# Kernel optimization log

Hardware: AMD Instinct MI355X
Metric: run time of the kernel (lower is better)

The kernel has to match this reference:

```python
import jax, jax.numpy as jnp
import numpy as np

# Dimensions matching init_kwargs
B, T, F = 256, 512, 128
COH_PTS, BULK_PTS, OUT_LEN = 64, 128, 6
COH_SIZE = 2 * COH_PTS            # fc11 out
IN_BULK = F + COH_PTS             # fc12 in
BULK_SIZE = 3 * BULK_PTS          # fc12 out

# Material constants (Turon cohesive bilinear law + J2 plasticity w/ linear hardening)
DELTA0, DELTAF = 0.01, 0.1        # damage onset / final equivalent jump
E_MOD, NU = 1.0e3, 0.3
G_MOD = E_MOD / (2.0 * (1.0 + NU))
SIG_Y, HARD = 10.0, 100.0
EPS = 1e-12
LEAKY_SLOPE = 0.01


def _plane_stress_D():
    c = E_MOD / (1.0 - NU * NU)
    return jnp.array([[c, c * NU, 0.0],
                      [c * NU, c, 0.0],
                      [0.0, 0.0, c * (1.0 - NU) / 2.0]], dtype=jnp.float32)


def setup_inputs() -> dict:
    key = jax.random.key(0)
    k_x, k_w11, k_b11, k_w12, k_w2 = jax.random.split(key, 5)
    scale11 = 1.0 / np.sqrt(F)
    scale12 = 1.0 / np.sqrt(IN_BULK)
    scale2 = 1.0 / np.sqrt(BULK_SIZE)
    return {
        "x": jax.random.normal(k_x, (B, T, F), dtype=jnp.float32),
        "W11": jax.random.normal(k_w11, (COH_SIZE, F), dtype=jnp.float32) * scale11,
        "b11": jax.random.normal(k_b11, (COH_SIZE,), dtype=jnp.float32) * scale11,
        "W12": jax.random.normal(k_w12, (BULK_SIZE, IN_BULK), dtype=jnp.float32) * scale12,
        "W2": jax.random.normal(k_w2, (OUT_LEN, BULK_SIZE), dtype=jnp.float32) * scale2,
    }


def reference(x, W11, b11, W12, W2):
    b, t, f = x.shape
    coh_pts = W11.shape[0] // 2
    bulk_pts = W12.shape[0] // 3
    D = _plane_stress_D()

    # fc11 (leaky-relu linear) is history-free -> vectorize over all timesteps
    jumps = jax.nn.leaky_relu(jnp.einsum('btf,cf->btc', x, W11) + b11,
                              LEAKY_SLOPE).reshape(b, t, coh_pts, 2)

    def step(carry, inp):
        dmg, ep = carry                      # [b, coh_pts], [b, bulk_pts]
        x_t, jump_t = inp                    # [b, f], [b, coh_pts, 2]

        # --- Turon cohesive update: monotone bilinear damage on equivalent jump ---
        jn = jax.nn.relu(jump_t[..., 0])     # tension-only normal jump
        js = jump_t[..., 1]
        delta = jnp.sqrt(jn * jn + js * js + EPS)
        d_new = jnp.clip(DELTAF * (delta - DELTA0)
                         / (jnp.maximum(delta, EPS) * (DELTAF - DELTA0)), 0.0, 1.0)
        dmg = jnp.maximum(dmg, d_new)        # commit: damage never heals

        # --- midini = cat(input, damages) -> fc12 (no bias) ---
        midini = jnp.concatenate([x_t, dmg], axis=-1)          # [b, f+coh_pts]
        strain = (midini @ W12.T).reshape(b, bulk_pts, 3)       # [b, bulk_pts, 3]

        # --- J2 plasticity (plane stress, radial return, linear hardening) ---
        sig_tr = jnp.einsum('bpi,ji->bpj', strain, D)           # trial stress
        sxx, syy, txy = sig_tr[..., 0], sig_tr[..., 1], sig_tr[..., 2]
        seq = jnp.sqrt(sxx * sxx - sxx * syy + syy * syy + 3.0 * txy * txy + EPS)
        fyield = seq - (SIG_Y + HARD * ep)
        dep = jnp.where(fyield > 0.0, fyield / (3.0 * G_MOD + HARD), 0.0)
        ep = ep + dep                                           # commit history
        scale = jnp.where(fyield > 0.0, (SIG_Y + HARD * ep) / seq, 1.0)
        sig = sig_tr * scale[..., None]

        # --- fc2 (softLayer: linear no bias + softplus) ---
        out_t = jax.nn.softplus(sig.reshape(b, -1) @ W2.T)      # [b, out_len]
        return (dmg, ep), out_t

    carry0 = (jnp.zeros((b, coh_pts), jnp.float32),
              jnp.zeros((b, bulk_pts), jnp.float32))
    _, out = jax.lax.scan(step, carry0,
                          (jnp.swapaxes(x, 0, 1), jnp.swapaxes(jumps, 0, 1)))
    return jnp.swapaxes(out, 0, 1)           # [b, t, out_len]
```

## Files before the change

kernel.cpp:

```cpp
#include <hip/hip_runtime.h>
#include <hip/hip_bf16.h>
#include <math.h>

#define NB 256
#define NT 512
#define NF 128
#define NCOH 64
#define NIN 192
#define NBS 384
#define NROWS (NB*NT)

#define C11 1098.9010989010989f
#define C12 329.67032967032966f
#define C33 384.61538461538464f
#define H3G 1253.8461538461538f
#define HOVER 0.07975460122699386f

typedef __attribute__((ext_vector_type(8))) short bf16x8;
typedef __attribute__((ext_vector_type(4))) float f32x4;
typedef __attribute__((ext_vector_type(8))) unsigned short ushort8v;
typedef __attribute__((ext_vector_type(4))) unsigned short ushort4v;

#define WAITCNT_VM(N) __builtin_amdgcn_s_waitcnt(0x0F70 | ((N) & 15) | (((N) >> 4) << 14))

#define PS ((size_t)NROWS * 32)
__device__ unsigned short g_Ahi[6 * PS];
__device__ unsigned short g_Bres[2 * NBS * NIN];
__device__ unsigned short g_W11res[32768];

static __device__ __forceinline__ unsigned short f2bf(float v) {
    __hip_bfloat16 h = __float2bfloat16(v);
    return *reinterpret_cast<unsigned short*>(&h);
}
static __device__ __forceinline__ float bf2f(unsigned short u) {
    unsigned int x = ((unsigned int)u) << 16;
    return *reinterpret_cast<float*>(&x);
}
static __device__ __forceinline__ void async_copy16(const void* g, void* l) {
    __builtin_amdgcn_global_load_lds(
        (const __attribute__((address_space(1))) unsigned int*)g,
        (__attribute__((address_space(3))) unsigned int*)l, 16, 0, 0);
}

__global__ __launch_bounds__(256) void k0_w12(const float* __restrict__ W12)
{
    const int idx = blockIdx.x * 256 + threadIdx.x;
    const int e    = idx & 7;
    const int l    = (idx >> 3) & 63;
    const int nf   = (idx >> 9) & 3;
    const int part = (idx >> 11) & 1;
    const int kc   = (idx >> 12) % 6;
    const int nblk = idx / 24576;
    const int n = nblk * 64 + nf * 16 + (l & 15);
    const int k = kc * 32 + (l >> 4) * 8 + e;
    const int p = n / 3, j = n - 3 * p;
    const float* w = W12 + (size_t)(3 * p) * NIN;
    float v;
    if (j == 0)      v = C11 * w[k]           + C12 * w[NIN + k];
    else if (j == 1) v = C12 * w[k]           + C11 * w[NIN + k];
    else             v = C33 * w[2 * NIN + k];
    unsigned short h = f2bf(v);
    g_Bres[idx] = part ? f2bf(v - bf2f(h)) : h;
}

__global__ __launch_bounds__(256) void k0b_w11(const float* __restrict__ W11)
{
    const int idx = blockIdx.x * 256 + threadIdx.x;
    const int e    = idx & 7;
    const int l    = (idx >> 3) & 63;
    const int nf   = (idx >> 9) & 7;
    const int part = (idx >> 12) & 1;
    const int kc   = idx >> 13;
    const int n = nf * 16 + (l & 15);
    const int k = kc * 32 + (l >> 4) * 8 + e;
    const float v = W11[(size_t)n * NF + k];
    unsigned short h = f2bf(v);
    g_W11res[idx] = part ? f2bf(v - bf2f(h)) : h;
}

__global__ __launch_bounds__(256) void k1_fc11(
    const float* __restrict__ x, const float* __restrict__ b11,
    unsigned short* __restrict__ dnT)
{
    __shared__ unsigned short Ws[32768];

    const int tid = threadIdx.x;
    const int lane = tid & 63, w = tid >> 6;
    const int fr = lane & 15, fq = lane >> 4;
    const int xbase = blockIdx.x * 128 + w * 32;

#pragma unroll
    for (int i = 0; i < 16; ++i)
        async_copy16((const char*)g_W11res + tid * 16 + i * 4096,
                     (char*)Ws + tid * 16 + i * 4096);

    f32x4 acc[8][2];
#pragma unroll
    for (int q = 0; q < 8; ++q)
#pragma unroll
        for (int f = 0; f < 2; ++f) acc[q][f] = (f32x4){0.f, 0.f, 0.f, 0.f};

    WAITCNT_VM(0);
    __builtin_amdgcn_s_barrier();

#pragma unroll
    for (int kc = 0; kc < 4; ++kc) {
        bf16x8 ah[2], al[2];
#pragma unroll
        for (int f = 0; f < 2; ++f) {
            const int row = xbase + f * 16 + fr;
            const float* xs = x + (size_t)row * NF + kc * 32 + fq * 8;
            float4 v0 = ((const float4*)xs)[0];
            float4 v1 = ((const float4*)xs)[1];
            float v[8] = {v0.x, v0.y, v0.z, v0.w, v1.x, v1.y, v1.z, v1.w};
            ushort8v h, lo;
#pragma unroll
            for (int i = 0; i < 8; ++i) {
                h[i]  = f2bf(v[i]);
                lo[i] = f2bf(v[i] - bf2f(h[i]));
            }
            *(ushort8v*)(g_Ahi + (size_t)kc * PS + (size_t)row * 32 + fq * 8) = h;
            ah[f] = *reinterpret_cast<bf16x8*>(&h);
            al[f] = *reinterpret_cast<bf16x8*>(&lo);
        }
#pragma unroll
        for (int q = 0; q < 8; ++q) {
            bf16x8 wh = *(const bf16x8*)&Ws[(kc * 16 + q) * 512 + lane * 8];
            bf16x8 wl = *(const bf16x8*)&Ws[(kc * 16 + 8 + q) * 512 + lane * 8];
#pragma unroll
            for (int f = 0; f < 2; ++f) {
                acc[q][f] = __builtin_amdgcn_mfma_f32_16x16x32_bf16(
                    wh, ah[f], acc[q][f], 0, 0, 0);
                acc[q][f] = __builtin_amdgcn_mfma_f32_16x16x32_bf16(
                    wl, ah[f], acc[q][f], 0, 0, 0);
                acc[q][f] = __builtin_amdgcn_mfma_f32_16x16x32_bf16(
                    wh, al[f], acc[q][f], 0, 0, 0);
            }
        }
    }

#pragma unroll
    for (int q = 0; q < 8; ++q) {
        float4 bv = *(const float4*)(b11 + q * 16 + fq * 4);
#pragma unroll
        for (int f = 0; f < 2; ++f) {
            const int xrow = xbase + f * 16 + fr;
            float z[4] = {acc[q][f][0] + bv.x, acc[q][f][1] + bv.y,
                          acc[q][f][2] + bv.z, acc[q][f][3] + bv.w};
#pragma unroll
            for (int pr = 0; pr < 2; ++pr) {
                float jn = fmaxf(z[2 * pr], 0.0f);
                float zs = z[2 * pr + 1];
                float js = (zs > 0.0f) ? zs : 0.01f * zs;
                float delta = sqrtf(jn * jn + js * js + 1e-12f);
                float dn = 0.1f * (delta - 0.01f) / (fmaxf(delta, 1e-12f) * 0.09f);
                dn = fminf(fmaxf(dn, 0.0f), 1.0f);
                dnT[(size_t)(q * 8 + fq * 2 + pr) * NROWS + xrow] = f2bf(dn);
            }
        }
    }
}

__global__ __launch_bounds__(64) void k2a(const unsigned short* __restrict__ dnT,
                                          float* __restrict__ totals)
{
    const int b = blockIdx.x >> 3, seg = blockIdx.x & 7;
    const int c = threadIdx.x;
    const ushort8v* p = (const ushort8v*)(dnT + (size_t)c * NROWS + b * NT + seg * 64);
    float m = 0.0f;
#pragma unroll
    for (int g = 0; g < 8; ++g) {
        ushort8v v = p[g];
#pragma unroll
        for (int i = 0; i < 8; ++i) m = fmaxf(m, bf2f(v[i]));
    }
    totals[(size_t)(b * 8 + seg) * 64 + c] = m;
}

__global__ __launch_bounds__(64) void k2b(const unsigned short* __restrict__ dnT,
                                          const float* __restrict__ totals)
{
    const int b = blockIdx.x >> 3, seg = blockIdx.x & 7;
    const int c = threadIdx.x;
    float carry = 0.0f;
    for (int s = 0; s < seg; ++s)
        carry = fmaxf(carry, totals[(size_t)(b * 8 + s) * 64 + c]);
    const ushort8v* p = (const ushort8v*)(dnT + (size_t)c * NROWS + b * NT + seg * 64);
    unsigned short* ah = g_Ahi + (size_t)(4 + (c >> 5)) * PS
                       + (size_t)(b * NT + seg * 64) * 32 + (c & 31);
    float m = carry;
#pragma unroll
    for (int g = 0; g < 8; ++g) {
        ushort8v v = p[g];
#pragma unroll
        for (int i = 0; i < 8; ++i) {
            m = fmaxf(m, bf2f(v[i]));
            ah[(size_t)(g * 8 + i) * 32] = f2bf(m);
        }
    }
}

__global__ __launch_bounds__(256, 3) void k3_mfma(unsigned short* __restrict__ sigT)
{
    __shared__ unsigned short Bs[24576];

    const int tid = threadIdx.x;
    const int lane = tid & 63, w = tid >> 6;
    const int id = blockIdx.x;
    const int sw = (id & 7) * 384 + (id >> 3);
    const int nblk = sw % 6;
    const int m0 = (sw / 6) * 256;
    const int n0 = nblk * 64;
    const int wm = w * 64;
    const int fr = lane & 15, fq = lane >> 4;

    const size_t abase = (size_t)(m0 + wm + fr) * 32 + fq * 8;

    bf16x8 a0[4], a1[4];
#pragma unroll
    for (int mi = 0; mi < 4; ++mi)
        a0[mi] = *(const bf16x8*)(g_Ahi + abase + mi * 512);

    {
        const char* bsrc = (const char*)g_Bres + (size_t)nblk * 49152;
#pragma unroll
        for (int i = 0; i < 12; ++i)
            async_copy16(bsrc + tid * 16 + i * 4096, (char*)Bs + tid * 16 + i * 4096);
    }
    WAITCNT_VM(0);
    __builtin_amdgcn_s_barrier();

    f32x4 acc[4][4];
#pragma unroll
    for (int mi = 0; mi < 4; ++mi)
#pragma unroll
        for (int ni = 0; ni < 4; ++ni) acc[mi][ni] = (f32x4){0.f, 0.f, 0.f, 0.f};

#pragma unroll
    for (int c = 0; c < 6; ++c) {
        bf16x8* acur = (c & 1) ? a1 : a0;
        bf16x8* anxt = (c & 1) ? a0 : a1;
        if (c < 5) {
#pragma unroll
            for (int mi = 0; mi < 4; ++mi)
                anxt[mi] = *(const bf16x8*)(g_Ahi + (size_t)(c + 1) * PS
                                            + abase + mi * 512);
        }
        bf16x8 bh[4], bl[4];
#pragma unroll
        for (int ni = 0; ni < 4; ++ni) {
            bh[ni] = *(const bf16x8*)&Bs[((c * 8 + ni) << 9) + lane * 8];
            bl[ni] = *(const bf16x8*)&Bs[((c * 8 + 4 + ni) << 9) + lane * 8];
        }
#pragma unroll
        for (int mi = 0; mi < 4; ++mi)
#pragma unroll
            for (int ni = 0; ni < 4; ++ni) {
                acc[mi][ni] = __builtin_amdgcn_mfma_f32_16x16x32_bf16(
                    acur[mi], bh[ni], acc[mi][ni], 0, 0, 0);
                acc[mi][ni] = __builtin_amdgcn_mfma_f32_16x16x32_bf16(
                    acur[mi], bl[ni], acc[mi][ni], 0, 0, 0);
            }
    }

    const int b_idx = m0 >> 9;
    const int tbase = (m0 & 511) + wm + fq * 4;
#pragma unroll
    for (int mi = 0; mi < 4; ++mi)
#pragma unroll
        for (int ni = 0; ni < 4; ++ni) {
            const int col = n0 + ni * 16 + fr;
            ushort4v h;
#pragma unroll
            for (int r = 0; r < 4; ++r) h[r] = f2bf(acc[mi][ni][r]);
            *(ushort4v*)(sigT + (((size_t)(b_idx * NBS + col)) << 9)
                              + tbase + mi * 16) = h;
        }
}

#define PFD 8
__global__ __launch_bounds__(128) void k4_scan(
    const unsigned short* __restrict__ sigT, unsigned short* __restrict__ uT)
{
    const int b = blockIdx.x;
    const int p = threadIdx.x;
    const ushort8v* sx = (const ushort8v*)(sigT + (((size_t)(b * NBS + 3 * p    )) << 9));
    const ushort8v* sy = (const ushort8v*)(sigT + (((size_t)(b * NBS + 3 * p + 1)) << 9));
    const ushort8v* sz = (const ushort8v*)(sigT + (((size_t)(b * NBS + 3 * p + 2)) << 9));
    ushort8v* uo = (ushort8v*)(uT + (((size_t)(b * 128 + p)) << 9));

    ushort8v px[PFD], py[PFD], pz[PFD];
#pragma unroll
    for (int g = 0; g < PFD; ++g) { px[g] = sx[g]; py[g] = sy[g]; pz[g] = sz[g]; }

    float u = 10.0f;
#pragma unroll 8
    for (int g = 0; g < 64 - PFD; ++g) {
        const int sl = g & (PFD - 1);
        ushort8v vx = px[sl], vy = py[sl], vz = pz[sl];
        px[sl] = sx[g + PFD]; py[sl] = sy[g + PFD]; pz[sl] = sz[g + PFD];
        ushort8v ov;
#pragma unroll
        for (int i = 0; i < 8; ++i) {
            float sxx = bf2f(vx[i]), syy = bf2f(vy[i]), txy = bf2f(vz[i]);
            float e = sxx*sxx - sxx*syy + syy*syy + 3.0f*txy*txy + 1e-12f;
            float seq = sqrtf(e);
            u = fmaf(fmaxf(seq - u, 0.0f), HOVER, u);
            ov[i] = f2bf(u);
        }
        uo[g] = ov;
    }
#pragma unroll
    for (int g = 64 - PFD; g < 64; ++g) {
        const int sl = g & (PFD - 1);
        ushort8v vx = px[sl], vy = py[sl], vz = pz[sl];
        ushort8v ov;
#pragma unroll
        for (int i = 0; i < 8; ++i) {
            float sxx = bf2f(vx[i]), syy = bf2f(vy[i]), txy = bf2f(vz[i]);
            float e = sxx*sxx - sxx*syy + syy*syy + 3.0f*txy*txy + 1e-12f;
            float seq = sqrtf(e);
            u = fmaf(fmaxf(seq - u, 0.0f), HOVER, u);
            ov[i] = f2bf(u);
        }
        uo[g] = ov;
    }
}

__global__ __launch_bounds__(256) void k5_out(
    const unsigned short* __restrict__ sigT, const unsigned short* __restrict__ uT,
    const float* __restrict__ W2, float* __restrict__ out)
{
    __shared__ float W2s[6][NBS];
    const int tid = threadIdx.x;
    for (int i = tid; i < 6 * NBS; i += 256) W2s[i / NBS][i % NBS] = W2[i];
    __syncthreads();

    const int b = blockIdx.x >> 1;
    const int t = (blockIdx.x & 1) * 256 + tid;
    const unsigned short* sb = sigT + (((size_t)b * NBS) << 9) + t;
    const unsigned short* ub = uT + (((size_t)b * 128) << 9) + t;

    float acc[6] = {0, 0, 0, 0, 0, 0};
#pragma unroll 4
    for (int p = 0; p < 128; ++p) {
        float sxx = bf2f(sb[(size_t)(3 * p    ) << 9]);
        float syy = bf2f(sb[(size_t)(3 * p + 1) << 9]);
        float txy = bf2f(sb[(size_t)(3 * p + 2) << 9]);
        float u   = bf2f(ub[(size_t)p << 9]);
        float e = sxx*sxx - sxx*syy + syy*syy + 3.0f*txy*txy + 1e-12f;
        float scale = fminf(1.0f, u * rsqrtf(e));
        float fx = sxx * scale, fy = syy * scale, fz = txy * scale;
#pragma unroll
        for (int o = 0; o < 6; ++o) {
            acc[o] = fmaf(fx, W2s[o][3 * p    ], acc[o]);
            acc[o] = fmaf(fy, W2s[o][3 * p + 1], acc[o]);
            acc[o] = fmaf(fz, W2s[o][3 * p + 2], acc[o]);
        }
    }

    float* op = out + ((size_t)(b * NT + t)) * 6;
#pragma unroll
    for (int o = 0; o < 6; ++o) {
        float z = acc[o];
        op[o] = fmaxf(z, 0.0f) + log1pf(expf(-fabsf(z)));
    }
}

extern "C" void kernel_launch(void* const* d_in, const int* in_sizes, int n_in,
                              void* d_out, int out_size, void* d_ws, size_t ws_size,
                              hipStream_t stream)
{
    const float* x   = (const float*)d_in[0];
    const float* W11 = (const float*)d_in[1];
    const float* b11 = (const float*)d_in[2];
    const float* W12 = (const float*)d_in[3];
    const float* W2  = (const float*)d_in[4];
    float* out = (float*)d_out;

    unsigned short* dnT = (unsigned short*)d_ws;
    unsigned short* uT = (unsigned short*)d_ws;
    unsigned short* sigT = (unsigned short*)((char*)d_ws + (size_t)NROWS * NCOH * sizeof(float));
    float* totals = (float*)((char*)d_ws + (size_t)128 * 1024 * 1024);

    k0_w12<<<(2 * NBS * NIN) / 256, 256, 0, stream>>>(W12);
    k0b_w11<<<128, 256, 0, stream>>>(W11);
    k1_fc11<<<NROWS / 128, 256, 0, stream>>>(x, b11, dnT);
    k2a<<<NB * 8, 64, 0, stream>>>(dnT, totals);
    k2b<<<NB * 8, 64, 0, stream>>>(dnT, totals);
    k3_mfma<<<3072, 256, 0, stream>>>(sigT);
    k4_scan<<<NB, 128, 0, stream>>>(sigT, uT);
    k5_out<<<NROWS / 256, 256, 0, stream>>>(sigT, uT, W2, out);
}
```

Measured before the change: 271.2 us.

## Fuse plasticity scan with output layer and stage GEMM stores through LDS

Merges the scan and output kernels into one 512-thread block per batch. The per-point yield-stress history is kept in a swizzled 128KB LDS buffer instead of being written to and re-read from global memory. The MFMA kernel also transposes its tile through shared memory so each lane writes 16-byte coalesced rows of sigT instead of scattered 8-byte stores. The trade-offs are that only 256 blocks run, the scan uses just 128 of 512 threads while the other 384 wait at the barrier, and W2 is now read from global/cache rather than LDS.

After: 308.1 us. 13.6% more time.

```diff
diff --git a/kernel.cpp b/kernel.cpp
--- a/kernel.cpp
+++ b/kernel.cpp
@@ -263,99 +263,110 @@
             }
     }
 
+    __syncthreads();
+    unsigned short* T = Bs;
+#pragma unroll
+    for (int mi = 0; mi < 4; ++mi)
+#pragma unroll
+        for (int ni = 0; ni < 4; ++ni) {
+            const int cIdx = ni * 16 + fr;
+            const int tloc = wm + mi * 16 + fq * 4;
+            ushort4v h;
+#pragma unroll
+            for (int r = 0; r < 4; ++r) h[r] = f2bf(acc[mi][ni][r]);
+            *(ushort4v*)&T[cIdx * 272 + tloc] = h;
+        }
+    __syncthreads();
+
     const int b_idx = m0 >> 9;
-    const int tbase = (m0 & 511) + wm + fq * 4;
-#pragma unroll
-    for (int mi = 0; mi < 4; ++mi)
-#pragma unroll
-        for (int ni = 0; ni < 4; ++ni) {
-            const int col = n0 + ni * 16 + fr;
-            ushort4v h;
-#pragma unroll
-            for (int r = 0; r < 4; ++r) h[r] = f2bf(acc[mi][ni][r]);
-            *(ushort4v*)(sigT + (((size_t)(b_idx * NBS + col)) << 9)
-                              + tbase + mi * 16) = h;
-        }
+    const int tq = lane & 31, c2 = lane >> 5;
+    const size_t colbase = (((size_t)(b_idx * NBS + n0)) << 9) + (m0 & 511);
+#pragma unroll
+    for (int it = 0; it < 8; ++it) {
+        const int cc = w * 16 + it * 2 + c2;
+        ushort8v v = *(const ushort8v*)&T[cc * 272 + tq * 8];
+        *(ushort8v*)(sigT + colbase + ((size_t)cc << 9) + tq * 8) = v;
+    }
 }
 
 #define PFD 8
-__global__ __launch_bounds__(128) void k4_scan(
-    const unsigned short* __restrict__ sigT, unsigned short* __restrict__ uT)
-{
+__global__ __launch_bounds__(512) void k45(
+    const unsigned short* __restrict__ sigT, const float* __restrict__ W2,
+    float* __restrict__ out)
+{
+    __shared__ unsigned short Ul[512 * 128];
+
+    const int tid = threadIdx.x;
     const int b = blockIdx.x;
-    const int p = threadIdx.x;
-    const ushort8v* sx = (const ushort8v*)(sigT + (((size_t)(b * NBS + 3 * p    )) << 9));
-    const ushort8v* sy = (const ushort8v*)(sigT + (((size_t)(b * NBS + 3 * p + 1)) << 9));
-    const ushort8v* sz = (const ushort8v*)(sigT + (((size_t)(b * NBS + 3 * p + 2)) << 9));
-    ushort8v* uo = (ushort8v*)(uT + (((size_t)(b * 128 + p)) << 9));
-
-    ushort8v px[PFD], py[PFD], pz[PFD];
-#pragma unroll
-    for (int g = 0; g < PFD; ++g) { px[g] = sx[g]; py[g] = sy[g]; pz[g] = sz[g]; }
-
-    float u = 10.0f;
+
+    if (tid < 128) {
+        const int p = tid;
+        const int pc = (p >> 3) << 3;
+        const int pw = p & 7;
+        const ushort8v* sx = (const ushort8v*)(sigT + (((size_t)(b * NBS + 3 * p    )) << 9));
+        const ushort8v* sy = (const ushort8v*)(sigT + (((size_t)(b * NBS + 3 * p + 1)) << 9));
+        const ushort8v* sz = (const ushort8v*)(sigT + (((size_t)(b * NBS + 3 * p + 2)) << 9));
+
+        ushort8v px[PFD], py[PFD], pz[PFD];
+#pragma unroll
+        for (int g = 0; g < PFD; ++g) { px[g] = sx[g]; py[g] = sy[g]; pz[g] = sz[g]; }
+
+        float u = 10.0f;
 #pragma unroll 8
-    for (int g = 0; g < 64 - PFD; ++g) {
-        const int sl = g & (PFD - 1);
-        ushort8v vx = px[sl], vy = py[sl], vz = pz[sl];
-        px[sl] = sx[g + PFD]; py[sl] = sy[g + PFD]; pz[sl] = sz[g + PFD];
-        ushort8v ov;
+        for (int g = 0; g < 64 - PFD; ++g) {
+            const int sl = g & (PFD - 1);
+            ushort8v vx = px[sl], vy = py[sl], vz = pz[sl];
+            px[sl] = sx[g + PFD]; py[sl] = sy[g + PFD]; pz[sl] = sz[g + PFD];
+#pragma unroll
+            for (int i = 0; i < 8; ++i) {
+                float sxx = bf2f(vx[i]), syy = bf2f(vy[i]), txy = bf2f(vz[i]);
+                float e = sxx*sxx - sxx*syy + syy*syy + 3.0f*txy*txy + 1e-12f;
+                float seq = sqrtf(e);
+                u = fmaf(fmaxf(seq - u, 0.0f), HOVER, u);
+                const int t = g * 8 + i;
+                Ul[t * 128 + (pc ^ ((t & 15) << 3)) + pw] = f2bf(u);
+            }
+        }
+#pragma unroll
+        for (int g = 64 - PFD; g < 64; ++g) {
+            const int sl = g & (PFD - 1);
+            ushort8v vx = px[sl], vy = py[sl], vz = pz[sl];
+#pragma unroll
+            for (int i = 0; i < 8; ++i) {
+                float sxx = bf2f(vx[i]), syy = bf2f(vy[i]), txy = bf2f(vz[i]);
+                float e = sxx*sxx - sxx*syy + syy*syy + 3.0f*txy*txy + 1e-12f;
+                float seq = sqrtf(e);
+                u = fmaf(fmaxf(seq - u, 0.0f), HOVER, u);
+                const int t = g * 8 + i;
+                Ul[t * 128 + (pc ^ ((t & 15) << 3)) + pw] = f2bf(u);
+            }
+        }
+    }
+    __syncthreads();
+
+    const int t = tid;
+    const unsigned short* sb = sigT + (((size_t)(b * NBS)) << 9) + t;
+
+    float acc[6] = {0, 0, 0, 0, 0, 0};
+#pragma unroll 2
+    for (int c = 0; c < 16; ++c) {
+        ushort8v uu = *(const ushort8v*)&Ul[t * 128 + ((c << 3) ^ ((t & 15) << 3))];
 #pragma unroll
         for (int i = 0; i < 8; ++i) {
-            float sxx = bf2f(vx[i]), syy = bf2f(vy[i]), txy = bf2f(vz[i]);
+            const int p = c * 8 + i;
+            float sxx = bf2f(sb[(size_t)(3 * p    ) << 9]);
+            float syy = bf2f(sb[(size_t)(3 * p + 1) << 9]);
+            float txy = bf2f(sb[(size_t)(3 * p + 2) << 9]);
+            float u   = bf2f(uu[i]);
             float e = sxx*sxx - sxx*syy + syy*syy + 3.0f*txy*txy + 1e-12f;
-            float seq = sqrtf(e);
-            u = fmaf(fmaxf(seq - u, 0.0f), HOVER, u);
-            ov[i] = f2bf(u);
-        }
-        uo[g] = ov;
-    }
-#pragma unroll
-    for (int g = 64 - PFD; g < 64; ++g) {
-        const int sl = g & (PFD - 1);
-        ushort8v vx = px[sl], vy = py[sl], vz = pz[sl];
-        ushort8v ov;
-#pragma unroll
-        for (int i = 0; i < 8; ++i) {
-            float sxx = bf2f(vx[i]), syy = bf2f(vy[i]), txy = bf2f(vz[i]);
-            float e = sxx*sxx - sxx*syy + syy*syy + 3.0f*txy*txy + 1e-12f;
-            float seq = sqrtf(e);
-            u = fmaf(fmaxf(seq - u, 0.0f), HOVER, u);
-            ov[i] = f2bf(u);
-        }
-        uo[g] = ov;
-    }
-}
-
-__global__ __launch_bounds__(256) void k5_out(
-    const unsigned short* __restrict__ sigT, const unsigned short* __restrict__ uT,
-    const float* __restrict__ W2, float* __restrict__ out)
-{
-    __shared__ float W2s[6][NBS];
-    const int tid = threadIdx.x;
-    for (int i = tid; i < 6 * NBS; i += 256) W2s[i / NBS][i % NBS] = W2[i];
-    __syncthreads();
-
-    const int b = blockIdx.x >> 1;
-    const int t = (blockIdx.x & 1) * 256 + tid;
-    const unsigned short* sb = sigT + (((size_t)b * NBS) << 9) + t;
-    const unsigned short* ub = uT + (((size_t)b * 128) << 9) + t;
-
-    float acc[6] = {0, 0, 0, 0, 0, 0};
-#pragma unroll 4
-    for (int p = 0; p < 128; ++p) {
-        float sxx = bf2f(sb[(size_t)(3 * p    ) << 9]);
-        float syy = bf2f(sb[(size_t)(3 * p + 1) << 9]);
-        float txy = bf2f(sb[(size_t)(3 * p + 2) << 9]);
-        float u   = bf2f(ub[(size_t)p << 9]);
-        float e = sxx*sxx - sxx*syy + syy*syy + 3.0f*txy*txy + 1e-12f;
-        float scale = fminf(1.0f, u * rsqrtf(e));
-        float fx = sxx * scale, fy = syy * scale, fz = txy * scale;
-#pragma unroll
-        for (int o = 0; o < 6; ++o) {
-            acc[o] = fmaf(fx, W2s[o][3 * p    ], acc[o]);
-            acc[o] = fmaf(fy, W2s[o][3 * p + 1], acc[o]);
-            acc[o] = fmaf(fz, W2s[o][3 * p + 2], acc[o]);
+            float scale = fminf(1.0f, u * rsqrtf(e));
+            float fx = sxx * scale, fy = syy * scale, fz = txy * scale;
+#pragma unroll
+            for (int o = 0; o < 6; ++o) {
+                acc[o] = fmaf(fx, W2[o * NBS + 3 * p    ], acc[o]);
+                acc[o] = fmaf(fy, W2[o * NBS + 3 * p + 1], acc[o]);
+                acc[o] = fmaf(fz, W2[o * NBS + 3 * p + 2], acc[o]);
+            }
         }
     }
 
@@ -379,7 +390,6 @@
     float* out = (float*)d_out;
 
     unsigned short* dnT = (unsigned short*)d_ws;
-    unsigned short* uT = (unsigned short*)d_ws;
     unsigned short* sigT = (unsigned short*)((char*)d_ws + (size_t)NROWS * NCOH * sizeof(float));
     float* totals = (float*)((char*)d_ws + (size_t)128 * 1024 * 1024);
 
@@ -389,6 +399,5 @@
     k2a<<<NB * 8, 64, 0, stream>>>(dnT, totals);
     k2b<<<NB * 8, 64, 0, stream>>>(dnT, totals);
     k3_mfma<<<3072, 256, 0, stream>>>(sigT);
-    k4_scan<<<NB, 128, 0, stream>>>(sigT, uT);
-    k5_out<<<NROWS / 256, 256, 0, stream>>>(sigT, uT, W2, out);
-}
+    k45<<<NB, 512, 0, stream>>>(sigT, W2, out);
+}
```
